# Performance work log

Measured on AMD Instinct MI355X. Metric: run time of the kernel, lower is better.

## Reference

```python
import jax, jax.numpy as jnp
import numpy as np

B, L, C = 2048, 2048, 16
F = L // 2                 # num_freqs = 1024
H = 4 * F                  # multi_factor * num_freqs = 4096
P = int(len(np.unique(L // np.arange(1, F + 1))))  # n patch sizes = 88
SCALE = 0.02
NOISE_EPS = 0.01


def setup_inputs() -> dict:
    key = jax.random.key(0)
    ks = jax.random.split(key, 10)
    return {
        "x": jax.random.normal(ks[0], (B, L, C), jnp.float32),
        "w_start": SCALE * jax.random.normal(ks[1], (C, 1), jnp.float32),
        "b_start": SCALE * jax.random.normal(ks[2], (1,), jnp.float32),
        "w1": SCALE * jax.random.normal(ks[3], (2, F, H), jnp.float32),
        "b1": SCALE * jax.random.normal(ks[4], (2, H), jnp.float32),
        "w2": SCALE * jax.random.normal(ks[5], (2, H, F), jnp.float32),
        "b2": SCALE * jax.random.normal(ks[6], (2, F), jnp.float32),
        "w_gate": SCALE * jax.random.normal(ks[7], (F, P), jnp.float32),
        "w_noise": SCALE * jax.random.normal(ks[8], (F, P), jnp.float32),
        "noise_z": jax.random.normal(ks[9], (B, P), jnp.float32),
        "top_k": 3,
    }


def reference(x, w_start, b_start, w1, b1, w2, b2, w_gate, w_noise, noise_z, top_k):
    # start_fc: [B, L, C] -> [B, L, 1] -> [B, 1, L]
    v = (jnp.einsum("blc,co->blo", x, w_start) + b_start).transpose(0, 2, 1)
    # rfft (ortho), drop DC bin -> [B, 1, F] complex
    xf = jnp.fft.rfft(v, axis=-1, norm="ortho")[:, :, 1:]
    xr, xi = jnp.real(xf), jnp.imag(xf)
    # complex 2-layer MLP in frequency domain
    o1r = jax.nn.relu(jnp.einsum("bdi,io->bdo", xr, w1[0]) - jnp.einsum("bdi,io->bdo", xi, w1[1]) + b1[0])
    o1i = jax.nn.relu(jnp.einsum("bdi,io->bdo", xi, w1[0]) + jnp.einsum("bdi,io->bdo", xr, w1[1]) + b1[1])
    o2r = jnp.einsum("bdo,of->bdf", o1r, w2[0]) - jnp.einsum("bdo,of->bdf", o1i, w2[1]) + b2[0]
    o2i = jnp.einsum("bdo,of->bdf", o1i, w2[0]) + jnp.einsum("bdo,of->bdf", o1r, w2[1]) + b2[1]
    amp = jnp.sqrt(o2r * o2r + o2i * o2i)[:, 0, :]  # [B, F]
    # router logits with (training) noise injection
    clean_logits = amp @ w_gate                      # [B, P]
    noise_std = jax.nn.softplus(amp @ w_noise) + NOISE_EPS
    logits = clean_logits + noise_z * noise_std
    # top-k -> softmax over top-k -> scatter into sparse gates
    top_w, top_i = jax.lax.top_k(logits, top_k)
    top_w = jax.nn.softmax(top_w, axis=-1)
    rows = jnp.arange(logits.shape[0])[:, None]
    gates = jnp.zeros_like(logits).at[rows, top_i].set(top_w)
    return gates
```

## Files before the change

### kernel.cpp

```cpp
#include <hip/hip_runtime.h>
#include <hip/hip_bf16.h>
#include <math.h>

#define B_DIM 2048
#define L_DIM 2048
#define F_DIM 1024
#define H_DIM 4096
#define P_DIM 88

typedef unsigned short u16;
typedef short bf16x8 __attribute__((ext_vector_type(8)));
typedef float f32x4 __attribute__((ext_vector_type(4)));

__device__ __forceinline__ u16 f2bf(float x) {
    unsigned u = __float_as_uint(x);
    return (u16)((u + 0x7fffu + ((u >> 16) & 1u)) >> 16);
}
__device__ __forceinline__ float bf2f(u16 h) {
    return __uint_as_float(((unsigned)h) << 16);
}

__device__ __forceinline__ void gload_lds16(const void* g, void* l) {
    unsigned loff = (unsigned)(uintptr_t)l;
    __builtin_amdgcn_global_load_lds(
        reinterpret_cast<const __attribute__((address_space(1))) void*>(
            reinterpret_cast<uintptr_t>(g)),
        reinterpret_cast<__attribute__((address_space(3))) void*>(loff),
        16, 0, 0);
}

__device__ __forceinline__ void conv_body(
    const float* __restrict__ w, u16* __restrict__ BT, int Kc, int Nh,
    int k0, int n0, int tx, int ty, float (*t0s)[33], float (*t1s)[33])
{
    const float* w0 = w;
    const float* w1b = w + (size_t)Kc * Nh;

#pragma unroll
    for (int i = 0; i < 4; i++) {
        int k = k0 + ty + 8 * i;
        t0s[ty + 8 * i][tx] = w0[(size_t)k * Nh + n0 + tx];
        t1s[ty + 8 * i][tx] = w1b[(size_t)k * Nh + n0 + tx];
    }
    __syncthreads();

    size_t K4 = 4 * (size_t)Kc;
    int k = k0 + tx;
#pragma unroll
    for (int i = 0; i < 4; i++) {
        int nl = ty + 8 * i;
        int n = n0 + nl;
        float br = t0s[tx][nl];
        float bi = t1s[tx][nl];
        u16 brh = f2bf(br); u16 brl = f2bf(br - bf2f(brh));
        float nbi = -bi;
        u16 nih = f2bf(nbi); u16 nil = f2bf(nbi - bf2f(nih));
        u16 pih = f2bf(bi);  u16 pil = f2bf(bi - bf2f(pih));
        u16* rowr = BT + (size_t)n * K4;
        rowr[0 * Kc + k] = brh; rowr[1 * Kc + k] = brl;
        rowr[2 * Kc + k] = nih; rowr[3 * Kc + k] = nil;
        u16* rowi = BT + (size_t)(Nh + n) * K4;
        rowi[0 * Kc + k] = pih; rowi[1 * Kc + k] = pil;
        rowi[2 * Kc + k] = brh; rowi[3 * Kc + k] = brl;
    }
}

__global__ __launch_bounds__(256) void prep_kernel(
    const float* __restrict__ x, const float* __restrict__ w_start,
    const float* __restrict__ b_start, u16* __restrict__ A1,
    const float* __restrict__ w1, u16* __restrict__ BT1,
    const float* __restrict__ w2, u16* __restrict__ BT2)
{
    __shared__ float re[2048];
    __shared__ float im[2048];
    __shared__ float twr[1024];
    __shared__ float twi[1024];
    __shared__ float t0s[32][33];
    __shared__ float t1s[32][33];

    const int tid = threadIdx.x;

    if (blockIdx.x < 1024) {
        int b = blockIdx.x;
        const size_t row0 = (size_t)(2 * b) * 2048;

        const float4* wp = (const float4*)w_start;
        float4 w0 = wp[0], w1v = wp[1], w2v = wp[2], w3 = wp[3];
        float bs = b_start[0];

        for (int i = tid; i < 1024; i += 256) {
            float ang = -6.283185307179586f * ((float)i / 2048.0f);
            sincosf(ang, &twi[i], &twr[i]);
        }

        for (int l = tid; l < 2048; l += 256) {
            const float4* xp0 = (const float4*)(x + (row0 + l) * 16);
            const float4* xp1 = (const float4*)(x + (row0 + 2048 + l) * 16);
            float4 a0 = xp0[0], a1 = xp0[1], a2 = xp0[2], a3 = xp0[3];
            float4 c0 = xp1[0], c1 = xp1[1], c2 = xp1[2], c3 = xp1[3];
            float va = bs, vb = bs;
            va += a0.x * w0.x + a0.y * w0.y + a0.z * w0.z + a0.w * w0.w;
            va += a1.x * w1v.x + a1.y * w1v.y + a1.z * w1v.z + a1.w * w1v.w;
            va += a2.x * w2v.x + a2.y * w2v.y + a2.z * w2v.z + a2.w * w2v.w;
            va += a3.x * w3.x + a3.y * w3.y + a3.z * w3.z + a3.w * w3.w;
            vb += c0.x * w0.x + c0.y * w0.y + c0.z * w0.z + c0.w * w0.w;
            vb += c1.x * w1v.x + c1.y * w1v.y + c1.z * w1v.z + c1.w * w1v.w;
            vb += c2.x * w2v.x + c2.y * w2v.y + c2.z * w2v.z + c2.w * w2v.w;
            vb += c3.x * w3.x + c3.y * w3.y + c3.z * w3.z + c3.w * w3.w;
            unsigned j = __brev((unsigned)l) >> 21;
            re[j] = va;
            im[j] = vb;
        }
        __syncthreads();

        for (int s = 1; s <= 11; s++) {
            int half = 1 << (s - 1);
            for (int t = tid; t < 1024; t += 256) {
                int j = t & (half - 1);
                int base = (t >> (s - 1)) << s;
                int idx = j << (11 - s);
                float wr = twr[idx], wi = twi[idx];
                int i0 = base + j, i1 = i0 + half;
                float br = re[i1], bi = im[i1];
                float tr = br * wr - bi * wi;
                float ti = br * wi + bi * wr;
                float ar = re[i0], ai = im[i0];
                re[i0] = ar + tr; im[i0] = ai + ti;
                re[i1] = ar - tr; im[i1] = ai - ti;
            }
            __syncthreads();
        }

        const float sc = 0.5f * 0.022097086912079612f;
        u16* r0 = A1 + (size_t)(2 * b) * 4096;
        u16* r1 = r0 + 4096;
        for (int t = tid; t < 1024; t += 256) {
            int k = t + 1;
            int nk = 2048 - k;
            float Zr = re[k], Zi = im[k], Yr = re[nk], Yi = im[nk];
            float Ar = (Zr + Yr) * sc;
            float Ai = (Zi - Yi) * sc;
            float Br = (Zi + Yi) * sc;
            float Bi = (Yr - Zr) * sc;
            u16 h, lo;
            h = f2bf(Ar); lo = f2bf(Ar - bf2f(h)); r0[t] = h; r0[1024 + t] = lo;
            h = f2bf(Ai); lo = f2bf(Ai - bf2f(h)); r0[2048 + t] = h; r0[3072 + t] = lo;
            h = f2bf(Br); lo = f2bf(Br - bf2f(h)); r1[t] = h; r1[1024 + t] = lo;
            h = f2bf(Bi); lo = f2bf(Bi - bf2f(h)); r1[2048 + t] = h; r1[3072 + t] = lo;
        }
    } else if (blockIdx.x < 5120) {
        int bid = blockIdx.x - 1024;
        int k0 = (bid & 31) * 32;
        int n0 = (bid >> 5) * 32;
        conv_body(w1, BT1, F_DIM, H_DIM, k0, n0, tid & 31, tid >> 5, t0s, t1s);
    } else {
        int bid = blockIdx.x - 5120;
        int k0 = (bid & 127) * 32;
        int n0 = (bid >> 7) * 32;
        conv_body(w2, BT2, H_DIM, F_DIM, k0, n0, tid & 31, tid >> 5, t0s, t1s);
    }
}

__global__ __launch_bounds__(256) void conv_bt_kernel(
    const float* __restrict__ w, u16* __restrict__ BT, int Kc, int Nh)
{
    __shared__ float t0[32][33];
    __shared__ float t1[32][33];
    conv_body(w, BT, Kc, Nh, blockIdx.x * 32, blockIdx.y * 32,
              threadIdx.x, threadIdx.y, t0, t1);
}

extern __shared__ char smem8p[];

template <int EPI, int SWZ, int PRIO>
__global__ __launch_bounds__(1024, 4) void gemm8p(
    const u16* __restrict__ A, const u16* __restrict__ B,
    const float* __restrict__ biasL, const float* __restrict__ biasR,
    u16* __restrict__ OutU, float* __restrict__ P01, float* __restrict__ P23,
    int Kc, int KcLog, int NH, int nt)
{
    char* ldsA = smem8p;
    char* ldsB = smem8p + 65536;

    const int tid = threadIdx.x;
    const int w = tid >> 6, lane = tid & 63;
    const int wr = w >> 2, wc = w & 3;
    const int fr = lane & 15, kb = lane >> 4;

    int bx, by, z;
    if (SWZ == 1) {
        int b = blockIdx.x;
        int xcd = b & 7, idx = b >> 3;
        bx = 4 * xcd + (idx & 3);
        by = idx >> 2;
        z = 0;
    } else if (SWZ == 2) {
        int b = blockIdx.x;
        by = b & 7;
        int s = b >> 3;
        bx = s & 7;
        z = s >> 3;
    } else {
        bx = blockIdx.x; by = blockIdx.y; z = blockIdx.z;
    }
    const int n0 = bx * 256, m0 = by * 256;
    const size_t K4 = 4 * (size_t)Kc;

    const int srow = tid >> 2;
    const int lk8 = (((tid & 3) ^ ((tid >> 3) & 3))) * 8;
    const int wb = w * 1024;
    const int laneOff = fr * 64 + ((kb ^ ((fr >> 1) & 3)) << 4);

    f32x4 acc[4][4];
#pragma unroll
    for (int i = 0; i < 4; i++)
#pragma unroll
        for (int j = 0; j < 4; j++)
            acc[i][j] = (f32x4){0.f, 0.f, 0.f, 0.f};

    const int t0 = z * nt, te = t0 + nt;

    auto colA = [&](int t) {
        int k0 = t << 5;
        int seg = k0 >> KcLog, kk = k0 & (Kc - 1);
        int r3 = seg >= 3 ? seg - 3 : seg;
        int bs = seg >= 3 ? 2 : 0;
        return (bs + (r3 == 1 ? 1 : 0)) * Kc + kk;
    };
    auto colB = [&](int t) {
        int k0 = t << 5;
        int seg = k0 >> KcLog, kk = k0 & (Kc - 1);
        int r3 = seg >= 3 ? seg - 3 : seg;
        int bs = seg >= 3 ? 2 : 0;
        return (bs + (r3 == 2 ? 1 : 0)) * Kc + kk;
    };
    auto stageA = [&](int t) {
        const u16* src = A + (size_t)(m0 + srow) * K4 + colA(t) + lk8;
        gload_lds16(src, ldsA + (t & 3) * 16384 + wb);
    };
    auto stageB = [&](int t) {
        const u16* src = B + (size_t)(n0 + srow) * K4 + colB(t) + lk8;
        gload_lds16(src, ldsB + (t & 3) * 16384 + wb);
    };
    auto aBase = [&](int t) -> const char* {
        return ldsA + (t & 3) * 16384 + wr * 4096 + laneOff;
    };
    auto bBase = [&](int t) -> const char* {
        return ldsB + (t & 3) * 16384 + wc * 4096 + laneOff;
    };

    stageA(t0); stageB(t0);
    if (t0 + 1 < te) { stageA(t0 + 1); stageB(t0 + 1); }
    if (t0 + 2 < te) { stageA(t0 + 2); stageB(t0 + 2); }
    if (t0 + 2 < te)      asm volatile("s_waitcnt vmcnt(4)" ::: "memory");
    else if (t0 + 1 < te) asm volatile("s_waitcnt vmcnt(2)" ::: "memory");
    else                  asm volatile("s_waitcnt vmcnt(0)" ::: "memory");
    asm volatile("s_barrier" ::: "memory");

    bf16x8 a0, a1, b0, b1, b2, b3;
    {
        const char* aS = aBase(t0);
        const char* bS = bBase(t0);
        a0 = *(const bf16x8*)(aS + 0 * 1024);
        a1 = *(const bf16x8*)(aS + 1 * 1024);
        b0 = *(const bf16x8*)(bS + 0 * 1024);
        b1 = *(const bf16x8*)(bS + 1 * 1024);
        b2 = *(const bf16x8*)(bS + 2 * 1024);
        b3 = *(const bf16x8*)(bS + 3 * 1024);
    }

    for (int t = t0; t < te; ++t) {
        const bool haveNext = (t + 1 < te);

        if (t + 3 < te) { stageA(t + 3); stageB(t + 3); }

        const char* aS = aBase(t);
        bf16x8 c0 = *(const bf16x8*)(aS + 2 * 1024);
        bf16x8 c1 = *(const bf16x8*)(aS + 3 * 1024);

        if (PRIO) __builtin_amdgcn_s_setprio(1);
        acc[0][0] = __builtin_amdgcn_mfma_f32_16x16x32_bf16(a0, b0, acc[0][0], 0, 0, 0);
        acc[0][1] = __builtin_amdgcn_mfma_f32_16x16x32_bf16(a0, b1, acc[0][1], 0, 0, 0);
        acc[0][2] = __builtin_amdgcn_mfma_f32_16x16x32_bf16(a0, b2, acc[0][2], 0, 0, 0);
        acc[0][3] = __builtin_amdgcn_mfma_f32_16x16x32_bf16(a0, b3, acc[0][3], 0, 0, 0);
        acc[1][0] = __builtin_amdgcn_mfma_f32_16x16x32_bf16(a1, b0, acc[1][0], 0, 0, 0);
        acc[1][1] = __builtin_amdgcn_mfma_f32_16x16x32_bf16(a1, b1, acc[1][1], 0, 0, 0);
        acc[1][2] = __builtin_amdgcn_mfma_f32_16x16x32_bf16(a1, b2, acc[1][2], 0, 0, 0);
        acc[1][3] = __builtin_amdgcn_mfma_f32_16x16x32_bf16(a1, b3, acc[1][3], 0, 0, 0);
        if (PRIO) __builtin_amdgcn_s_setprio(0);

        if (t + 3 < te)      asm volatile("s_waitcnt vmcnt(4)" ::: "memory");
        else if (t + 2 < te) asm volatile("s_waitcnt vmcnt(2)" ::: "memory");
        else                 asm volatile("s_waitcnt vmcnt(0)" ::: "memory");
        asm volatile("s_barrier" ::: "memory");

        if (haveNext) {
            const char* aN = aBase(t + 1);
            a0 = *(const bf16x8*)(aN + 0 * 1024);
            a1 = *(const bf16x8*)(aN + 1 * 1024);
        }

        if (PRIO) __builtin_amdgcn_s_setprio(1);
        acc[2][0] = __builtin_amdgcn_mfma_f32_16x16x32_bf16(c0, b0, acc[2][0], 0, 0, 0);
        acc[2][1] = __builtin_amdgcn_mfma_f32_16x16x32_bf16(c0, b1, acc[2][1], 0, 0, 0);
        acc[2][2] = __builtin_amdgcn_mfma_f32_16x16x32_bf16(c0, b2, acc[2][2], 0, 0, 0);
        acc[2][3] = __builtin_amdgcn_mfma_f32_16x16x32_bf16(c0, b3, acc[2][3], 0, 0, 0);
        acc[3][0] = __builtin_amdgcn_mfma_f32_16x16x32_bf16(c1, b0, acc[3][0], 0, 0, 0);
        acc[3][1] = __builtin_amdgcn_mfma_f32_16x16x32_bf16(c1, b1, acc[3][1], 0, 0, 0);
        acc[3][2] = __builtin_amdgcn_mfma_f32_16x16x32_bf16(c1, b2, acc[3][2], 0, 0, 0);
        acc[3][3] = __builtin_amdgcn_mfma_f32_16x16x32_bf16(c1, b3, acc[3][3], 0, 0, 0);
        if (PRIO) __builtin_amdgcn_s_setprio(0);

        if (haveNext) {
            const char* bN = bBase(t + 1);
            b0 = *(const bf16x8*)(bN + 0 * 1024);
            b1 = *(const bf16x8*)(bN + 1 * 1024);
            b2 = *(const bf16x8*)(bN + 2 * 1024);
            b3 = *(const bf16x8*)(bN + 3 * 1024);
        }
    }

    const int fq = kb;
#pragma unroll
    for (int nj = 0; nj < 4; nj++) {
        int n = n0 + wc * 64 + nj * 16 + fr;
        if (EPI == 0) {
            bool left = (n < NH);
            int nn = left ? n : (n - NH);
            float bias = left ? biasL[n] : biasR[nn];
#pragma unroll
            for (int mi = 0; mi < 4; mi++) {
                int mb = m0 + wr * 64 + mi * 16 + fq * 4;
#pragma unroll
                for (int r = 0; r < 4; r++) {
                    float val = fmaxf(acc[mi][nj][r] + bias, 0.f);
                    u16 h = f2bf(val);
                    u16 lo = f2bf(val - bf2f(h));
                    size_t rb = (size_t)(mb + r) * (4 * (size_t)NH);
                    if (left) { OutU[rb + nn] = h; OutU[rb + NH + nn] = lo; }
                    else { OutU[rb + 2 * (size_t)NH + nn] = h; OutU[rb + 3 * (size_t)NH + nn] = lo; }
                }
            }
        } else {
            const size_t PSZ = (size_t)2048 * 2048;
            float* Out = (z < 2) ? (P01 + (size_t)z * PSZ) : (P23 + (size_t)(z - 2) * PSZ);
#pragma unroll
            for (int mi = 0; mi < 4; mi++) {
                int mb = m0 + wr * 64 + mi * 16 + fq * 4;
#pragma unroll
                for (int r = 0; r < 4; r++)
                    Out[(size_t)(mb + r) * 2048 + n] = acc[mi][nj][r];
            }
        }
    }
}

__global__ __launch_bounds__(256) void router_kernel(
    const float* __restrict__ P01, const float* __restrict__ P23, int ZK,
    const float* __restrict__ b2,
    const float* __restrict__ w_gate, const float* __restrict__ w_noise,
    const float* __restrict__ noise_z, float* __restrict__ gates)
{
    __shared__ float s_amp[8][1024];
    __shared__ float s_dot[8][176];
    __shared__ float s_lg[8][88];
    __shared__ int   s_idx[8][3];
    __shared__ float s_val[8][3];

    const int tid = threadIdx.x;
    const int r0 = blockIdx.x * 8;
    const size_t PSZ = (size_t)2048 * 2048;

    for (int idx = tid; idx < 8 * 1024; idx += 256) {
        int row = idx >> 10, i = idx & 1023;
        size_t roff = (size_t)(r0 + row) * 2048;
        float orr = b2[i];
        float oii = b2[1024 + i];
        for (int zz = 0; zz < ZK; zz++) {
            const float* Pz = ((zz < 2) ? (P01 + (size_t)zz * PSZ)
                                        : (P23 + (size_t)(zz - 2) * PSZ)) + roff;
            orr += Pz[i];
            oii += Pz[1024 + i];
        }
        s_amp[row][i] = sqrtf(orr * orr + oii * oii);
    }
    __syncthreads();

    for (int idx = tid; idx < 8 * 176; idx += 256) {
        int row = idx / 176, c = idx % 176;
        const float* wcol = (c < 88) ? (w_gate + c) : (w_noise + (c - 88));
        float s = 0.f;
        const float4* av = (const float4*)s_amp[row];
        for (int k4 = 0; k4 < 256; k4++) {
            float4 a = av[k4];
            int k = k4 * 4;
            s = fmaf(a.x, wcol[(size_t)(k + 0) * 88], s);
            s = fmaf(a.y, wcol[(size_t)(k + 1) * 88], s);
            s = fmaf(a.z, wcol[(size_t)(k + 2) * 88], s);
            s = fmaf(a.w, wcol[(size_t)(k + 3) * 88], s);
        }
        s_dot[row][c] = s;
    }
    __syncthreads();

    for (int idx = tid; idx < 8 * 88; idx += 256) {
        int row = idx / 88, c = idx % 88;
        float cn = s_dot[row][88 + c];
        float ns = (cn > 20.f) ? cn : log1pf(expf(cn));
        ns += 0.01f;
        s_lg[row][c] = s_dot[row][c] + noise_z[(size_t)(r0 + row) * 88 + c] * ns;
    }
    __syncthreads();

    if (tid < 8) {
        int i0 = -1, i1 = -1, i2 = -1;
        float v0 = -1e30f, v1 = -1e30f, v2 = -1e30f;
        for (int i = 0; i < P_DIM; i++) {
            float t = s_lg[tid][i];
            if (t > v0) { v0 = t; i0 = i; }
        }
        for (int i = 0; i < P_DIM; i++) {
            if (i == i0) continue;
            float t = s_lg[tid][i];
            if (t > v1) { v1 = t; i1 = i; }
        }
        for (int i = 0; i < P_DIM; i++) {
            if (i == i0 || i == i1) continue;
            float t = s_lg[tid][i];
            if (t > v2) { v2 = t; i2 = i; }
        }
        s_idx[tid][0] = i0; s_idx[tid][1] = i1; s_idx[tid][2] = i2;
        s_val[tid][0] = v0; s_val[tid][1] = v1; s_val[tid][2] = v2;
    }
    __syncthreads();

    for (int idx = tid; idx < 8 * 88; idx += 256) {
        int row = idx / 88, c = idx % 88;
        float m = s_val[row][0];
        float e0 = expf(s_val[row][0] - m);
        float e1 = expf(s_val[row][1] - m);
        float e2 = expf(s_val[row][2] - m);
        float inv = 1.f / (e0 + e1 + e2);
        float g = 0.f;
        if (c == s_idx[row][0]) g = e0 * inv;
        else if (c == s_idx[row][1]) g = e1 * inv;
        else if (c == s_idx[row][2]) g = e2 * inv;
        gates[(size_t)(r0 + row) * 88 + c] = g;
    }
}

extern "C" void kernel_launch(void* const* d_in, const int* in_sizes, int n_in,
                              void* d_out, int out_size, void* d_ws, size_t ws_size,
                              hipStream_t stream)
{
    const float* x       = (const float*)d_in[0];
    const float* w_start = (const float*)d_in[1];
    const float* b_start = (const float*)d_in[2];
    const float* w1      = (const float*)d_in[3];
    const float* b1      = (const float*)d_in[4];
    const float* w2      = (const float*)d_in[5];
    const float* b2      = (const float*)d_in[6];
    const float* w_gate  = (const float*)d_in[7];
    const float* w_noise = (const float*)d_in[8];
    const float* noise_z = (const float*)d_in[9];
    float* gates = (float*)d_out;

    const size_t MB = 1024 * 1024;
    char* base = (char*)d_ws;

    hipFuncSetAttribute(reinterpret_cast<const void*>(&gemm8p<0, 1, 0>),
                        hipFuncAttributeMaxDynamicSharedMemorySize, 131072);
    hipFuncSetAttribute(reinterpret_cast<const void*>(&gemm8p<1, 2, 1>),
                        hipFuncAttributeMaxDynamicSharedMemorySize, 131072);

    if (ws_size >= (size_t)208 * MB) {
        u16*  BT1 = (u16*)base;
        u16*  A1  = (u16*)(base + 64 * MB);
        u16*  BT2 = (u16*)(base + 80 * MB);
        u16*  A2  = (u16*)(base + 144 * MB);
        float* P01 = (float*)base;
        float* P23 = (float*)(base + 32 * MB);

        prep_kernel<<<1024 + 4096 + 4096, 256, 0, stream>>>(
            x, w_start, b_start, A1, w1, BT1, w2, BT2);

        gemm8p<0, 1, 0><<<256, 1024, 131072, stream>>>(
            A1, BT1, b1, b1 + H_DIM, A2, nullptr, nullptr, F_DIM, 10, H_DIM, 192);

        gemm8p<1, 2, 1><<<64 * 4, 1024, 131072, stream>>>(
            A2, BT2, nullptr, nullptr, nullptr, P01, P23, H_DIM, 12, F_DIM, 192);

        router_kernel<<<B_DIM / 8, 256, 0, stream>>>(
            P01, P23, 4, b2, w_gate, w_noise, noise_z, gates);
    } else {
        u16*  A1  = (u16*)(base + 16 * MB);
        u16*  BT  = (u16*)(base + 32 * MB);
        u16*  A2  = (u16*)(base + 96 * MB);
        float* P01 = (float*)base;
        float* P23 = (float*)(base + 160 * MB);
        int ZK = (ws_size >= (size_t)192 * MB) ? 4 : 2;

        prep_kernel<<<1024 + 4096, 256, 0, stream>>>(
            x, w_start, b_start, A1, w1, BT, w2, BT );

        gemm8p<0, 1, 0><<<256, 1024, 131072, stream>>>(
            A1, BT, b1, b1 + H_DIM, A2, nullptr, nullptr, F_DIM, 10, H_DIM, 192);

        conv_bt_kernel<<<dim3(H_DIM / 32, F_DIM / 32), dim3(32, 8), 0, stream>>>(
            w2, BT, H_DIM, F_DIM);
        gemm8p<1, 2, 1><<<64 * ZK, 1024, 131072, stream>>>(
            A2, BT, nullptr, nullptr, nullptr, P01, P23, H_DIM, 12, F_DIM, 768 / ZK);

        router_kernel<<<B_DIM / 8, 256, 0, stream>>>(
            P01, P23, ZK, b2, w_gate, w_noise, noise_z, gates);
    }
}
```

Measured before the change: 574.6 us.

## Process two K-tiles per barrier in GEMM main loop and drop setprio

The GEMM main loop now handles two K-tiles per iteration, staging the next pair of tiles at once and synchronising with a single vmcnt(0) wait plus barrier per pair instead of per tile. The s_setprio priority template parameter is removed. The aim is to halve barrier and wait overhead, at the cost of shallower effective prefetch, since waits now drain all outstanding loads. It assumes an even tile count per block, which holds for the 192-tile launches used here.

```diff
diff --git a/kernel.cpp b/kernel.cpp
--- a/kernel.cpp
+++ b/kernel.cpp
@@ -172,7 +172,17 @@
 
 extern __shared__ char smem8p[];
 
-template <int EPI, int SWZ, int PRIO>
+#define MFMA8(I0, I1, A0, A1)                                                       \
+    acc[I0][0] = __builtin_amdgcn_mfma_f32_16x16x32_bf16(A0, b0, acc[I0][0], 0, 0, 0); \
+    acc[I0][1] = __builtin_amdgcn_mfma_f32_16x16x32_bf16(A0, b1, acc[I0][1], 0, 0, 0); \
+    acc[I0][2] = __builtin_amdgcn_mfma_f32_16x16x32_bf16(A0, b2, acc[I0][2], 0, 0, 0); \
+    acc[I0][3] = __builtin_amdgcn_mfma_f32_16x16x32_bf16(A0, b3, acc[I0][3], 0, 0, 0); \
+    acc[I1][0] = __builtin_amdgcn_mfma_f32_16x16x32_bf16(A1, b0, acc[I1][0], 0, 0, 0); \
+    acc[I1][1] = __builtin_amdgcn_mfma_f32_16x16x32_bf16(A1, b1, acc[I1][1], 0, 0, 0); \
+    acc[I1][2] = __builtin_amdgcn_mfma_f32_16x16x32_bf16(A1, b2, acc[I1][2], 0, 0, 0); \
+    acc[I1][3] = __builtin_amdgcn_mfma_f32_16x16x32_bf16(A1, b3, acc[I1][3], 0, 0, 0);
+
+template <int EPI, int SWZ>
 __global__ __launch_bounds__(1024, 4) void gemm8p(
     const u16* __restrict__ A, const u16* __restrict__ B,
     const float* __restrict__ biasL, const float* __restrict__ biasR,
@@ -250,11 +260,8 @@
     };
 
     stageA(t0); stageB(t0);
-    if (t0 + 1 < te) { stageA(t0 + 1); stageB(t0 + 1); }
-    if (t0 + 2 < te) { stageA(t0 + 2); stageB(t0 + 2); }
-    if (t0 + 2 < te)      asm volatile("s_waitcnt vmcnt(4)" ::: "memory");
-    else if (t0 + 1 < te) asm volatile("s_waitcnt vmcnt(2)" ::: "memory");
-    else                  asm volatile("s_waitcnt vmcnt(0)" ::: "memory");
+    stageA(t0 + 1); stageB(t0 + 1);
+    asm volatile("s_waitcnt vmcnt(0)" ::: "memory");
     asm volatile("s_barrier" ::: "memory");
 
     bf16x8 a0, a1, b0, b1, b2, b3;
@@ -269,50 +276,43 @@
         b3 = *(const bf16x8*)(bS + 3 * 1024);
     }
 
-    for (int t = t0; t < te; ++t) {
-        const bool haveNext = (t + 1 < te);
-
-        if (t + 3 < te) { stageA(t + 3); stageB(t + 3); }
+    for (int t = t0; t < te; t += 2) {
+        const bool more = (t + 2 < te);
+
+        if (more) { stageA(t + 2); stageB(t + 2); stageA(t + 3); stageB(t + 3); }
 
         const char* aS = aBase(t);
         bf16x8 c0 = *(const bf16x8*)(aS + 2 * 1024);
         bf16x8 c1 = *(const bf16x8*)(aS + 3 * 1024);
-
-        if (PRIO) __builtin_amdgcn_s_setprio(1);
-        acc[0][0] = __builtin_amdgcn_mfma_f32_16x16x32_bf16(a0, b0, acc[0][0], 0, 0, 0);
-        acc[0][1] = __builtin_amdgcn_mfma_f32_16x16x32_bf16(a0, b1, acc[0][1], 0, 0, 0);
-        acc[0][2] = __builtin_amdgcn_mfma_f32_16x16x32_bf16(a0, b2, acc[0][2], 0, 0, 0);
-        acc[0][3] = __builtin_amdgcn_mfma_f32_16x16x32_bf16(a0, b3, acc[0][3], 0, 0, 0);
-        acc[1][0] = __builtin_amdgcn_mfma_f32_16x16x32_bf16(a1, b0, acc[1][0], 0, 0, 0);
-        acc[1][1] = __builtin_amdgcn_mfma_f32_16x16x32_bf16(a1, b1, acc[1][1], 0, 0, 0);
-        acc[1][2] = __builtin_amdgcn_mfma_f32_16x16x32_bf16(a1, b2, acc[1][2], 0, 0, 0);
-        acc[1][3] = __builtin_amdgcn_mfma_f32_16x16x32_bf16(a1, b3, acc[1][3], 0, 0, 0);
-        if (PRIO) __builtin_amdgcn_s_setprio(0);
-
-        if (t + 3 < te)      asm volatile("s_waitcnt vmcnt(4)" ::: "memory");
-        else if (t + 2 < te) asm volatile("s_waitcnt vmcnt(2)" ::: "memory");
-        else                 asm volatile("s_waitcnt vmcnt(0)" ::: "memory");
-        asm volatile("s_barrier" ::: "memory");
-
-        if (haveNext) {
+        MFMA8(0, 1, a0, a1)
+
+        {
             const char* aN = aBase(t + 1);
             a0 = *(const bf16x8*)(aN + 0 * 1024);
             a1 = *(const bf16x8*)(aN + 1 * 1024);
         }
-
-        if (PRIO) __builtin_amdgcn_s_setprio(1);
-        acc[2][0] = __builtin_amdgcn_mfma_f32_16x16x32_bf16(c0, b0, acc[2][0], 0, 0, 0);
-        acc[2][1] = __builtin_amdgcn_mfma_f32_16x16x32_bf16(c0, b1, acc[2][1], 0, 0, 0);
-        acc[2][2] = __builtin_amdgcn_mfma_f32_16x16x32_bf16(c0, b2, acc[2][2], 0, 0, 0);
-        acc[2][3] = __builtin_amdgcn_mfma_f32_16x16x32_bf16(c0, b3, acc[2][3], 0, 0, 0);
-        acc[3][0] = __builtin_amdgcn_mfma_f32_16x16x32_bf16(c1, b0, acc[3][0], 0, 0, 0);
-        acc[3][1] = __builtin_amdgcn_mfma_f32_16x16x32_bf16(c1, b1, acc[3][1], 0, 0, 0);
-        acc[3][2] = __builtin_amdgcn_mfma_f32_16x16x32_bf16(c1, b2, acc[3][2], 0, 0, 0);
-        acc[3][3] = __builtin_amdgcn_mfma_f32_16x16x32_bf16(c1, b3, acc[3][3], 0, 0, 0);
-        if (PRIO) __builtin_amdgcn_s_setprio(0);
-
-        if (haveNext) {
+        MFMA8(2, 3, c0, c1)
+
+        {
             const char* bN = bBase(t + 1);
+            b0 = *(const bf16x8*)(bN + 0 * 1024);
+            b1 = *(const bf16x8*)(bN + 1 * 1024);
+            b2 = *(const bf16x8*)(bN + 2 * 1024);
+            b3 = *(const bf16x8*)(bN + 3 * 1024);
+            const char* aN = aBase(t + 1);
+            c0 = *(const bf16x8*)(aN + 2 * 1024);
+            c1 = *(const bf16x8*)(aN + 3 * 1024);
+        }
+        MFMA8(0, 1, a0, a1)
+        MFMA8(2, 3, c0, c1)
+
+        if (more) {
+            asm volatile("s_waitcnt vmcnt(0)" ::: "memory");
+            asm volatile("s_barrier" ::: "memory");
+            const char* aN = aBase(t + 2);
+            const char* bN = bBase(t + 2);
+            a0 = *(const bf16x8*)(aN + 0 * 1024);
+            a1 = *(const bf16x8*)(aN + 1 * 1024);
             b0 = *(const bf16x8*)(bN + 0 * 1024);
             b1 = *(const bf16x8*)(bN + 1 * 1024);
             b2 = *(const bf16x8*)(bN + 2 * 1024);
@@ -468,9 +468,9 @@
     const size_t MB = 1024 * 1024;
     char* base = (char*)d_ws;
 
-    hipFuncSetAttribute(reinterpret_cast<const void*>(&gemm8p<0, 1, 0>),
+    hipFuncSetAttribute(reinterpret_cast<const void*>(&gemm8p<0, 1>),
                         hipFuncAttributeMaxDynamicSharedMemorySize, 131072);
-    hipFuncSetAttribute(reinterpret_cast<const void*>(&gemm8p<1, 2, 1>),
+    hipFuncSetAttribute(reinterpret_cast<const void*>(&gemm8p<1, 2>),
                         hipFuncAttributeMaxDynamicSharedMemorySize, 131072);
 
     if (ws_size >= (size_t)208 * MB) {
@@ -484,10 +484,10 @@
         prep_kernel<<<1024 + 4096 + 4096, 256, 0, stream>>>(
             x, w_start, b_start, A1, w1, BT1, w2, BT2);
 
-        gemm8p<0, 1, 0><<<256, 1024, 131072, stream>>>(
+        gemm8p<0, 1><<<256, 1024, 131072, stream>>>(
             A1, BT1, b1, b1 + H_DIM, A2, nullptr, nullptr, F_DIM, 10, H_DIM, 192);
 
-        gemm8p<1, 2, 1><<<64 * 4, 1024, 131072, stream>>>(
+        gemm8p<1, 2><<<64 * 4, 1024, 131072, stream>>>(
             A2, BT2, nullptr, nullptr, nullptr, P01, P23, H_DIM, 12, F_DIM, 192);
 
         router_kernel<<<B_DIM / 8, 256, 0, stream>>>(
@@ -503,12 +503,12 @@
         prep_kernel<<<1024 + 4096, 256, 0, stream>>>(
             x, w_start, b_start, A1, w1, BT, w2, BT );
 
-        gemm8p<0, 1, 0><<<256, 1024, 131072, stream>>>(
+        gemm8p<0, 1><<<256, 1024, 131072, stream>>>(
             A1, BT, b1, b1 + H_DIM, A2, nullptr, nullptr, F_DIM, 10, H_DIM, 192);
 
         conv_bt_kernel<<<dim3(H_DIM / 32, F_DIM / 32), dim3(32, 8), 0, stream>>>(
             w2, BT, H_DIM, F_DIM);
-        gemm8p<1, 2, 1><<<64 * ZK, 1024, 131072, stream>>>(
+        gemm8p<1, 2><<<64 * ZK, 1024, 131072, stream>>>(
             A2, BT, nullptr, nullptr, nullptr, P01, P23, H_DIM, 12, F_DIM, 768 / ZK);
 
         router_kernel<<<B_DIM / 8, 256, 0, stream>>>(
```

After: 566.5 us, median of 2. About the same (-1.4%).
